# Kernel optimization log

Hardware: AMD Instinct MI355X
Metric: run time of the kernel (lower is better)

Reference implementation:

```python
import jax, jax.numpy as jnp
import numpy as np
import math

DIM = 128
K = 64
OUT = 256
N, H, W = 32, 64, 64
EPS = 1e-12  # F.normalize clamp


def _l2norm(v, axis):
    n = jnp.sqrt(jnp.sum(v * v, axis=axis, keepdims=True))
    return v / jnp.maximum(n, EPS)


def setup_inputs() -> dict:
    key = jax.random.key(0)
    ks = jax.random.split(key, 6)
    s = 1.0 / math.sqrt(DIM)
    x = jax.random.normal(ks[0], (N, DIM, H, W), dtype=jnp.float32)
    cluster_centers = jax.random.uniform(ks[1], (K, DIM), dtype=jnp.float32) * s
    conv_w = jax.random.normal(ks[2], (K, DIM), dtype=jnp.float32) * s  # 1x1 conv kernel squeezed
    conv_b = jax.random.normal(ks[3], (K,), dtype=jnp.float32) * s
    mlp_w = jax.random.normal(ks[4], (OUT, K * DIM), dtype=jnp.float32) * s / math.sqrt(K * DIM)
    mlp_b = jax.random.normal(ks[5], (OUT,), dtype=jnp.float32) * s
    return {"x": x, "cluster_centers": cluster_centers, "conv_w": conv_w,
            "conv_b": conv_b, "mlp_w": mlp_w, "mlp_b": mlp_b}


def reference(x, cluster_centers, conv_w, conv_b, mlp_w, mlp_b):
    n, c, h, w = x.shape
    xf = x.reshape(n, c, h * w)                                   # [N,C,P]
    # 1x1 conv == per-pixel matmul
    logits = jnp.einsum('kc,ncp->nkp', conv_w, xf) + conv_b[None, :, None]
    a = jax.nn.softmax(logits, axis=1)                            # softmax over clusters, [N,K,P]
    # VLAD via algebraic identity (same math as broadcast-subtract-sum):
    # sum_p a[n,k,p]*(x[n,c,p] - centers[k,c])
    vlad = jnp.einsum('nkp,ncp->nkc', a, xf) \
           - a.sum(axis=-1)[..., None] * cluster_centers[None]    # [N,K,C]
    vlad = _l2norm(vlad, axis=2)            # intra-normalization over C
    vlad = vlad.reshape(n, -1)              # [N, K*C]
    vlad = _l2norm(vlad, axis=1)
    vlad = vlad @ mlp_w.T + mlp_b           # [N, OUT]
    vlad = _l2norm(vlad, axis=1)
    return vlad
```

## Files before the change

kernel.cpp:

```cpp
#include <hip/hip_runtime.h>
#include <math.h>


#define N_IMG 32
#define C_DIM 128
#define P_PIX 4096
#define K_CL  64
#define OUT_D 256

#define CHUNKS 8
#define NSUB 4
#define PART_ROW 132
#define PART_BLK (K_CL * PART_ROW)

typedef __attribute__((ext_vector_type(8))) short bf16x8;
typedef __attribute__((ext_vector_type(4))) short bf16x4;
typedef __attribute__((ext_vector_type(4))) float f32x4;
typedef __attribute__((ext_vector_type(2))) unsigned u32x2;
typedef __attribute__((ext_vector_type(4))) unsigned u32x4;

__device__ __forceinline__ unsigned cvtpk(float a, float b) {
    unsigned r;
    asm("v_cvt_pk_bf16_f32 %0, %1, %2" : "=v"(r) : "v"(a), "v"(b));
    return r;
}
__device__ __forceinline__ unsigned short bf1(float a) {
    union { float f; unsigned u; } x; x.f = a;
    return (unsigned short)((x.u + 0x7FFFu + ((x.u >> 16) & 1u)) >> 16);
}

__device__ __forceinline__ f32x4 mfma16(bf16x8 a, bf16x8 b, f32x4 c) {
    return __builtin_amdgcn_mfma_f32_16x16x32_bf16(a, b, c, 0, 0, 0);
}

__device__ __forceinline__ u32x2 tr16(unsigned addr) {
    u32x2 d;
    asm volatile("ds_read_b64_tr_b16 %0, %1" : "=v"(d) : "v"(addr));
    return d;
}
__device__ __forceinline__ u32x2 tr16_o1024(unsigned addr) {
    u32x2 d;
    asm volatile("ds_read_b64_tr_b16 %0, %1 offset:1024" : "=v"(d) : "v"(addr));
    return d;
}

__device__ __forceinline__ void bar_lgkm() {
    __builtin_amdgcn_sched_barrier(0);
    asm volatile("s_waitcnt lgkmcnt(0)" ::: "memory");
    __builtin_amdgcn_s_barrier();
    __builtin_amdgcn_sched_barrier(0);
}

template<int CTRL>
__device__ __forceinline__ float dppmv(float v) {
    union { float f; int i; } u; u.f = v;
    u.i = __builtin_amdgcn_update_dpp(u.i, u.i, CTRL, 0xF, 0xF, false);
    return u.f;
}
__device__ __forceinline__ float rowmax16(float v) {
    v = fmaxf(v, dppmv<0xB1>(v));
    v = fmaxf(v, dppmv<0x4E>(v));
    v = fmaxf(v, dppmv<0x141>(v));
    v = fmaxf(v, dppmv<0x140>(v));
    return v;
}
__device__ __forceinline__ float rowsum16(float v) {
    v += dppmv<0xB1>(v);
    v += dppmv<0x4E>(v);
    v += dppmv<0x141>(v);
    v += dppmv<0x140>(v);
    return v;
}

__global__ __launch_bounds__(256, 1)
void k_vlad_mfma(const float* __restrict__ x, const float* __restrict__ conv_w,
                 const float* __restrict__ conv_b, float* __restrict__ part)
{
    __shared__ short xc_s[16384];
    __shared__ short a_s[8192];
    __shared__ short w_s[8192];
    __shared__ float asred[256];

    const int t   = threadIdx.x;
    const int w   = t >> 6;
    const int l   = t & 63;
    const int l15 = l & 15;
    const int lg  = l >> 4;
    const int n   = blockIdx.x >> 3;
    const int ch  = blockIdx.x & 7;
    const int pb0 = ch * 512;

    const unsigned xc_base = (unsigned)(unsigned long long)(void*)xc_s;
    const float LOG2E = 1.44269504f;

    const float* xr0 = x + ((long)n * C_DIM + 32 * w + l15) * P_PIX;
    const float* xr1 = xr0 + 16 * P_PIX;
    float4 raw[16];
#pragma unroll
    for (int h = 0; h < 2; ++h) {
        const float* xr = h ? xr1 : xr0;
#pragma unroll
        for (int ks = 0; ks < 4; ++ks) {
            const float* p = xr + pb0 + ks * 32 + lg * 8;
            raw[(h * 4 + ks) * 2 + 0] = *(const float4*)(p);
            raw[(h * 4 + ks) * 2 + 1] = *(const float4*)(p + 4);
        }
    }

    {
        const int k = t >> 2, quad = t & 3;
        const float* wr = conv_w + k * C_DIM + quad * 32;
#pragma unroll
        for (int j = 0; j < 4; ++j) {
            float4 a = *(const float4*)(wr + j * 8);
            float4 b = *(const float4*)(wr + j * 8 + 4);
            union { u32x4 u; bf16x8 v; } cv;
            cv.u.x = cvtpk(a.x * LOG2E, a.y * LOG2E);
            cv.u.y = cvtpk(a.z * LOG2E, a.w * LOG2E);
            cv.u.z = cvtpk(b.x * LOG2E, b.y * LOG2E);
            cv.u.w = cvtpk(b.z * LOG2E, b.w * LOG2E);
            const int g = quad * 4 + j;
            const unsigned off = (unsigned)(k * 256 + ((g * 16) ^ ((k & 7) << 4)));
            *(bf16x8*)((char*)w_s + off) = cv.v;
        }
    }
    float bias[4];
#pragma unroll
    for (int nt = 0; nt < 4; ++nt) bias[nt] = conv_b[nt * 16 + l15] * LOG2E;

    f32x4 acc2[4][2];
#pragma unroll
    for (int mt = 0; mt < 4; ++mt)
#pragma unroll
        for (int h = 0; h < 2; ++h)
            acc2[mt][h] = (f32x4){0.f, 0.f, 0.f, 0.f};
    float asum[4] = {0.f, 0.f, 0.f, 0.f};
    bf16x8 oct[2][4];

#pragma unroll
    for (int s = 0; s < NSUB; ++s) {
#pragma unroll
        for (int h = 0; h < 2; ++h)
#pragma unroll
            for (int ks = 0; ks < 4; ++ks) {
                const float4 A = raw[(h * 4 + ks) * 2];
                const float4 B = raw[(h * 4 + ks) * 2 + 1];
                union { u32x4 u; bf16x8 v; } cv;
                cv.u.x = cvtpk(A.x, A.y); cv.u.y = cvtpk(A.z, A.w);
                cv.u.z = cvtpk(B.x, B.y); cv.u.w = cvtpk(B.z, B.w);
                oct[h][ks] = cv.v;
            }
#pragma unroll
        for (int h = 0; h < 2; ++h)
#pragma unroll
            for (int ks = 0; ks < 4; ++ks) {
                const int c  = 32 * w + 16 * h + l15;
                const int pl = ks * 32 + lg * 8;
                const unsigned off = (unsigned)((c >> 2) * 1024 + (pl >> 4) * 128
                                                + (c & 3) * 32 + (pl & 15) * 2);
                *(bf16x8*)((char*)xc_s + off) = oct[h][ks];
            }
        if (s + 1 < NSUB) {
#pragma unroll
            for (int h = 0; h < 2; ++h) {
                const float* xr = h ? xr1 : xr0;
#pragma unroll
                for (int ks = 0; ks < 4; ++ks) {
                    const float* p = xr + pb0 + (s + 1) * 128 + ks * 32 + lg * 8;
                    raw[(h * 4 + ks) * 2 + 0] = *(const float4*)(p);
                    raw[(h * 4 + ks) * 2 + 1] = *(const float4*)(p + 4);
                }
            }
        }
        bar_lgkm();

        f32x4 acc1[2][4];
#pragma unroll
        for (int pt2 = 0; pt2 < 2; ++pt2)
#pragma unroll
            for (int nt = 0; nt < 4; ++nt)
                acc1[pt2][nt] = (f32x4){0.f, 0.f, 0.f, 0.f};
#pragma unroll
        for (int ks = 0; ks < 4; ++ks) {
            const unsigned ab = xc_base
                + (unsigned)((ks * 8 + lg * 2) * 1024 + l15 * 2);
            u32x2 t00 = tr16(ab + (2 * w + 0) * 128);
            u32x2 t01 = tr16_o1024(ab + (2 * w + 0) * 128);
            u32x2 t10 = tr16(ab + (2 * w + 1) * 128);
            u32x2 t11 = tr16_o1024(ab + (2 * w + 1) * 128);
            bf16x8 wfr[4];
#pragma unroll
            for (int nt = 0; nt < 4; ++nt) {
                const unsigned wb = (unsigned)((nt * 16 + l15) * 256
                    + ((ks * 64 + lg * 16) ^ ((l15 & 7) << 4)));
                wfr[nt] = *(const bf16x8*)((char*)w_s + wb);
            }
            asm volatile("s_waitcnt lgkmcnt(0)" ::: "memory");
            __builtin_amdgcn_sched_barrier(0);
            union { u32x4 u; bf16x8 v; } a0, a1;
            a0.u = (u32x4){t00.x, t00.y, t01.x, t01.y};
            a1.u = (u32x4){t10.x, t10.y, t11.x, t11.y};
#pragma unroll
            for (int nt = 0; nt < 4; ++nt) {
                acc1[0][nt] = mfma16(a0.v, wfr[nt], acc1[0][nt]);
                acc1[1][nt] = mfma16(a1.v, wfr[nt], acc1[1][nt]);
            }
        }

#pragma unroll
        for (int pt2 = 0; pt2 < 2; ++pt2) {
#pragma unroll
            for (int r = 0; r < 4; ++r) {
                float v0 = acc1[pt2][0][r] + bias[0];
                float v1 = acc1[pt2][1][r] + bias[1];
                float v2 = acc1[pt2][2][r] + bias[2];
                float v3 = acc1[pt2][3][r] + bias[3];
                float m = fmaxf(fmaxf(v0, v1), fmaxf(v2, v3));
                m = rowmax16(m);
                v0 = exp2f(v0 - m); v1 = exp2f(v1 - m);
                v2 = exp2f(v2 - m); v3 = exp2f(v3 - m);
                float sm = (v0 + v1) + (v2 + v3);
                sm = rowsum16(sm);
                const float inv = __builtin_amdgcn_rcpf(sm);
                v0 *= inv; v1 *= inv; v2 *= inv; v3 *= inv;
                asum[0] += v0; asum[1] += v1; asum[2] += v2; asum[3] += v3;
                acc1[pt2][0][r] = v0; acc1[pt2][1][r] = v1;
                acc1[pt2][2][r] = v2; acc1[pt2][3][r] = v3;
            }
        }
#pragma unroll
        for (int pt2 = 0; pt2 < 2; ++pt2) {
            const int pbyte = (2 * w + pt2) * 32 + lg * 8;
#pragma unroll
            for (int nt = 0; nt < 4; ++nt) {
                const int k = nt * 16 + l15;
                union { u32x2 u; bf16x4 v; } pk4;
                pk4.u.x = cvtpk(acc1[pt2][nt][0], acc1[pt2][nt][1]);
                pk4.u.y = cvtpk(acc1[pt2][nt][2], acc1[pt2][nt][3]);
                const unsigned off =
                    (unsigned)(k * 256 + (pbyte ^ ((k & 7) << 4)));
                *(bf16x4*)((char*)a_s + off) = pk4.v;
            }
        }
        bar_lgkm();

#pragma unroll
        for (int ks = 0; ks < 4; ++ks) {
            bf16x8 af[4];
#pragma unroll
            for (int mt = 0; mt < 4; ++mt) {
                const int k = mt * 16 + l15;
                const unsigned off = (unsigned)(k * 256
                    + ((ks * 64 + lg * 16) ^ ((k & 7) << 4)));
                af[mt] = *(const bf16x8*)((char*)a_s + off);
            }
#pragma unroll
            for (int mt = 0; mt < 4; ++mt)
#pragma unroll
                for (int h = 0; h < 2; ++h)
                    acc2[mt][h] = mfma16(af[mt], oct[h][ks], acc2[mt][h]);
        }
    }

    const long pbase = (long)blockIdx.x * PART_BLK;
#pragma unroll
    for (int mt = 0; mt < 4; ++mt)
#pragma unroll
        for (int h = 0; h < 2; ++h) {
            const int c = 32 * w + 16 * h + l15;
#pragma unroll
            for (int r = 0; r < 4; ++r) {
                const int k = mt * 16 + lg * 4 + r;
                part[pbase + (long)k * PART_ROW + c] = acc2[mt][h][r];
            }
        }
#pragma unroll
    for (int nt = 0; nt < 4; ++nt) {
        float a = asum[nt];
        a += __shfl_xor(a, 16);
        a += __shfl_xor(a, 32);
        if (lg == 0) asred[w * 64 + nt * 16 + l15] = a;
    }
    __syncthreads();
    if (t < 64) {
        float a = asred[t] + asred[64 + t] + asred[128 + t] + asred[192 + t];
        part[pbase + (long)t * PART_ROW + 128] = a;
    }
}

__global__ __launch_bounds__(128)
void k_reduce_norm(const float* __restrict__ part, const float* __restrict__ centers,
                   unsigned short* __restrict__ vn16, float* __restrict__ rsq)
{
    const int b = blockIdx.x;
    const int n = b >> 6, k = b & 63;
    const int c = threadIdx.x;
    float acc = 0.f, as = 0.f;
#pragma unroll
    for (int ch = 0; ch < CHUNKS; ++ch) {
        const float* p = part + ((long)(n * CHUNKS + ch) * PART_BLK + k * PART_ROW);
        acc += p[c];
        as  += p[128];
    }
    const float v = fmaf(-as, centers[k * C_DIM + c], acc);
    float sq = v * v;
#pragma unroll
    for (int m = 1; m < 64; m <<= 1) sq += __shfl_xor(sq, m);
    __shared__ float red[2];
    if ((c & 63) == 0) red[c >> 6] = sq;
    __syncthreads();
    const float total = red[0] + red[1];
    const float s = 1.0f / fmaxf(sqrtf(total), 1e-12f);
    vn16[(long)n * 8192 + k * C_DIM + c] = bf1(v * s);
    if (c == 0) rsq[n * K_CL + k] = total * s * s;
}

__global__ __launch_bounds__(256)
void k_mlp_mfma(const unsigned short* __restrict__ vn16,
                const float* __restrict__ mlp_w, float* __restrict__ part2)
{
    __shared__ short wt[8192];
    __shared__ short vt[8192];

    const int t  = threadIdx.x;
    const int og = blockIdx.x & 7;
    const int jc = blockIdx.x >> 3;
    const int j0 = jc * 256;

    {
        const int r = t >> 3, sub = t & 7;
        const float* wp = mlp_w + (long)(og * 32 + r) * 8192 + j0;
#pragma unroll
        for (int i = 0; i < 8; ++i) {
            const int jl = i * 32 + sub * 4;
            float4 a = *(const float4*)(wp + jl);
            union { u32x2 u; bf16x4 v; } cv;
            cv.u.x = cvtpk(a.x, a.y);
            cv.u.y = cvtpk(a.z, a.w);
            const unsigned off = (unsigned)(r * 512 + ((jl * 2) ^ ((r & 7) << 4)));
            *(bf16x4*)((char*)wt + off) = cv.v;
        }
    }
    {
        const int r = t >> 3, sub = t & 7;
        const unsigned short* vp = vn16 + (long)r * 8192 + j0;
#pragma unroll
        for (int i = 0; i < 4; ++i) {
            const int jl = i * 64 + sub * 8;
            bf16x8 v = *(const bf16x8*)(vp + jl);
            const unsigned off = (unsigned)(r * 512 + ((jl * 2) ^ ((r & 7) << 4)));
            *(bf16x8*)((char*)vt + off) = v;
        }
    }
    __syncthreads();

    const int w = t >> 6, l = t & 63, l15 = l & 15, lg = l >> 4;
    const int mt = w >> 1, ot = w & 1;
    f32x4 acc = (f32x4){0.f, 0.f, 0.f, 0.f};
#pragma unroll
    for (int kk = 0; kk < 8; ++kk) {
        const int rowa = mt * 16 + l15;
        const int rowb = ot * 16 + l15;
        const int jb = (kk * 32 + lg * 8) * 2;
        bf16x8 af = *(const bf16x8*)((char*)vt
                        + (unsigned)(rowa * 512 + (jb ^ ((rowa & 7) << 4))));
        bf16x8 bf = *(const bf16x8*)((char*)wt
                        + (unsigned)(rowb * 512 + (jb ^ ((rowb & 7) << 4))));
        acc = mfma16(af, bf, acc);
    }
#pragma unroll
    for (int r = 0; r < 4; ++r) {
        const int nn = mt * 16 + lg * 4 + r;
        const int oo = og * 32 + ot * 16 + l15;
        part2[(long)nn * 8192 + jc * 256 + oo] = acc[r];
    }
}

__global__ __launch_bounds__(1024)
void k_finalize(const float* __restrict__ part2, const float* __restrict__ mlp_b,
                const float* __restrict__ rsq, float* __restrict__ out)
{
    __shared__ float psum[4][256];
    __shared__ float red[4];
    const int n = blockIdx.x;
    const int t = threadIdx.x;
    const int o = t & 255, q = t >> 8;

    float acc = 0.f;
#pragma unroll
    for (int j = 0; j < 8; ++j)
        acc += part2[(long)n * 8192 + (q * 8 + j) * 256 + o];
    psum[q][o] = acc;
    __syncthreads();

    float y = 0.f;
    if (q == 0) {
        float g = 0.f;
#pragma unroll
        for (int i = 0; i < 16; ++i) {
            const float4 r = *(const float4*)&rsq[n * K_CL + i * 4];
            g += r.x + r.y + r.z + r.w;
        }
        const float s = 1.0f / fmaxf(sqrtf(g), 1e-12f);
        const float tot = psum[0][o] + psum[1][o] + psum[2][o] + psum[3][o];
        y = fmaf(tot * s, 1.0f, mlp_b[o]);
        float sq = y * y;
#pragma unroll
        for (int m = 1; m < 64; m <<= 1) sq += __shfl_xor(sq, m);
        if ((o & 63) == 0) red[o >> 6] = sq;
    }
    __syncthreads();
    if (q == 0) {
        const float tot2 = red[0] + red[1] + red[2] + red[3];
        out[n * OUT_D + o] = y / fmaxf(sqrtf(tot2), 1e-12f);
    }
}

extern "C" void kernel_launch(void* const* d_in, const int* in_sizes, int n_in,
                              void* d_out, int out_size, void* d_ws, size_t ws_size,
                              hipStream_t stream)
{
    const float* x       = (const float*)d_in[0];
    const float* centers = (const float*)d_in[1];
    const float* conv_w  = (const float*)d_in[2];
    const float* conv_b  = (const float*)d_in[3];
    const float* mlp_w   = (const float*)d_in[4];
    const float* mlp_b   = (const float*)d_in[5];

    float* ws = (float*)d_ws;
    float* part = ws;
    unsigned short* vn16 = (unsigned short*)(part + 256 * PART_BLK);
    float* rsq   = (float*)(vn16 + 32 * 8192);
    float* part2 = rsq + 2048;

    k_vlad_mfma<<<dim3(256), dim3(256), 0, stream>>>(x, conv_w, conv_b, part);
    k_reduce_norm<<<dim3(2048), dim3(128), 0, stream>>>(part, centers, vn16, rsq);
    k_mlp_mfma<<<dim3(256), dim3(256), 0, stream>>>(vn16, mlp_w, part2);
    k_finalize<<<dim3(32), dim3(1024), 0, stream>>>(part2, mlp_b, rsq, (float*)d_out);
}
```

Before: 38.06 us.

## Double wavefronts per block in VLAD kernel, halving per-wave channel and pixel work

The main VLAD kernel now runs 512 threads (8 waves) per block instead of 256. Each wave owns 16 channels and one 16-pixel tile rather than 32 channels and two tiles, so per-thread registers and MFMA chains shrink by half. The conv weight fragments are also loaded once into registers before the sub-chunk loop instead of being re-read from LDS every iteration. This is meant to raise latency hiding and occupancy for the global loads and MFMAs, at the cost of more waves contending at each barrier and higher register pressure from keeping the 16 preloaded weight fragments live.

```diff
diff --git a/kernel.cpp b/kernel.cpp
--- a/kernel.cpp
+++ b/kernel.cpp
@@ -72,14 +72,14 @@
     return v;
 }
 
-__global__ __launch_bounds__(256, 1)
+__global__ __launch_bounds__(512, 2)
 void k_vlad_mfma(const float* __restrict__ x, const float* __restrict__ conv_w,
                  const float* __restrict__ conv_b, float* __restrict__ part)
 {
     __shared__ short xc_s[16384];
     __shared__ short a_s[8192];
     __shared__ short w_s[8192];
-    __shared__ float asred[256];
+    __shared__ float asred[512];
 
     const int t   = threadIdx.x;
     const int w   = t >> 6;
@@ -93,25 +93,20 @@
     const unsigned xc_base = (unsigned)(unsigned long long)(void*)xc_s;
     const float LOG2E = 1.44269504f;
 
-    const float* xr0 = x + ((long)n * C_DIM + 32 * w + l15) * P_PIX;
-    const float* xr1 = xr0 + 16 * P_PIX;
-    float4 raw[16];
-#pragma unroll
-    for (int h = 0; h < 2; ++h) {
-        const float* xr = h ? xr1 : xr0;
-#pragma unroll
-        for (int ks = 0; ks < 4; ++ks) {
-            const float* p = xr + pb0 + ks * 32 + lg * 8;
-            raw[(h * 4 + ks) * 2 + 0] = *(const float4*)(p);
-            raw[(h * 4 + ks) * 2 + 1] = *(const float4*)(p + 4);
-        }
+    const float* xr0 = x + ((long)n * C_DIM + 16 * w + l15) * P_PIX;
+    float4 raw[8];
+#pragma unroll
+    for (int ks = 0; ks < 4; ++ks) {
+        const float* p = xr0 + pb0 + ks * 32 + lg * 8;
+        raw[ks * 2 + 0] = *(const float4*)(p);
+        raw[ks * 2 + 1] = *(const float4*)(p + 4);
     }
 
     {
-        const int k = t >> 2, quad = t & 3;
-        const float* wr = conv_w + k * C_DIM + quad * 32;
-#pragma unroll
-        for (int j = 0; j < 4; ++j) {
+        const int k = t >> 3, sub = t & 7;
+        const float* wr = conv_w + k * C_DIM + sub * 16;
+#pragma unroll
+        for (int j = 0; j < 2; ++j) {
             float4 a = *(const float4*)(wr + j * 8);
             float4 b = *(const float4*)(wr + j * 8 + 4);
             union { u32x4 u; bf16x8 v; } cv;
@@ -119,7 +114,7 @@
             cv.u.y = cvtpk(a.z * LOG2E, a.w * LOG2E);
             cv.u.z = cvtpk(b.x * LOG2E, b.y * LOG2E);
             cv.u.w = cvtpk(b.z * LOG2E, b.w * LOG2E);
-            const int g = quad * 4 + j;
+            const int g = sub * 2 + j;
             const unsigned off = (unsigned)(k * 256 + ((g * 16) ^ ((k & 7) << 4)));
             *(bf16x8*)((char*)w_s + off) = cv.v;
         }
@@ -128,115 +123,102 @@
 #pragma unroll
     for (int nt = 0; nt < 4; ++nt) bias[nt] = conv_b[nt * 16 + l15] * LOG2E;
 
-    f32x4 acc2[4][2];
-#pragma unroll
-    for (int mt = 0; mt < 4; ++mt)
-#pragma unroll
-        for (int h = 0; h < 2; ++h)
-            acc2[mt][h] = (f32x4){0.f, 0.f, 0.f, 0.f};
+    bar_lgkm();
+
+    bf16x8 wf[4][4];
+#pragma unroll
+    for (int nt = 0; nt < 4; ++nt)
+#pragma unroll
+        for (int ks = 0; ks < 4; ++ks) {
+            const unsigned wb = (unsigned)((nt * 16 + l15) * 256
+                + ((ks * 64 + lg * 16) ^ ((l15 & 7) << 4)));
+            wf[nt][ks] = *(const bf16x8*)((char*)w_s + wb);
+        }
+
+    f32x4 acc2[4];
+#pragma unroll
+    for (int mt = 0; mt < 4; ++mt) acc2[mt] = (f32x4){0.f, 0.f, 0.f, 0.f};
     float asum[4] = {0.f, 0.f, 0.f, 0.f};
-    bf16x8 oct[2][4];
+    bf16x8 oct[4];
 
 #pragma unroll
     for (int s = 0; s < NSUB; ++s) {
 #pragma unroll
-        for (int h = 0; h < 2; ++h)
+        for (int ks = 0; ks < 4; ++ks) {
+            const float4 A = raw[ks * 2];
+            const float4 B = raw[ks * 2 + 1];
+            union { u32x4 u; bf16x8 v; } cv;
+            cv.u.x = cvtpk(A.x, A.y); cv.u.y = cvtpk(A.z, A.w);
+            cv.u.z = cvtpk(B.x, B.y); cv.u.w = cvtpk(B.z, B.w);
+            oct[ks] = cv.v;
+        }
+#pragma unroll
+        for (int ks = 0; ks < 4; ++ks) {
+            const int c  = 16 * w + l15;
+            const int pl = ks * 32 + lg * 8;
+            const unsigned off = (unsigned)((c >> 2) * 1024 + (pl >> 4) * 128
+                                            + (c & 3) * 32 + (pl & 15) * 2);
+            *(bf16x8*)((char*)xc_s + off) = oct[ks];
+        }
+        if (s + 1 < NSUB) {
 #pragma unroll
             for (int ks = 0; ks < 4; ++ks) {
-                const float4 A = raw[(h * 4 + ks) * 2];
-                const float4 B = raw[(h * 4 + ks) * 2 + 1];
-                union { u32x4 u; bf16x8 v; } cv;
-                cv.u.x = cvtpk(A.x, A.y); cv.u.y = cvtpk(A.z, A.w);
-                cv.u.z = cvtpk(B.x, B.y); cv.u.w = cvtpk(B.z, B.w);
-                oct[h][ks] = cv.v;
+                const float* p = xr0 + pb0 + (s + 1) * 128 + ks * 32 + lg * 8;
+                raw[ks * 2 + 0] = *(const float4*)(p);
+                raw[ks * 2 + 1] = *(const float4*)(p + 4);
             }
-#pragma unroll
-        for (int h = 0; h < 2; ++h)
-#pragma unroll
-            for (int ks = 0; ks < 4; ++ks) {
-                const int c  = 32 * w + 16 * h + l15;
-                const int pl = ks * 32 + lg * 8;
-                const unsigned off = (unsigned)((c >> 2) * 1024 + (pl >> 4) * 128
-                                                + (c & 3) * 32 + (pl & 15) * 2);
-                *(bf16x8*)((char*)xc_s + off) = oct[h][ks];
-            }
-        if (s + 1 < NSUB) {
-#pragma unroll
-            for (int h = 0; h < 2; ++h) {
-                const float* xr = h ? xr1 : xr0;
-#pragma unroll
-                for (int ks = 0; ks < 4; ++ks) {
-                    const float* p = xr + pb0 + (s + 1) * 128 + ks * 32 + lg * 8;
-                    raw[(h * 4 + ks) * 2 + 0] = *(const float4*)(p);
-                    raw[(h * 4 + ks) * 2 + 1] = *(const float4*)(p + 4);
-                }
-            }
         }
         bar_lgkm();
 
-        f32x4 acc1[2][4];
-#pragma unroll
-        for (int pt2 = 0; pt2 < 2; ++pt2)
+        u32x2 trr[4][2];
+#pragma unroll
+        for (int ks = 0; ks < 4; ++ks) {
+            const unsigned ab = xc_base
+                + (unsigned)((ks * 8 + lg * 2) * 1024 + l15 * 2 + w * 128);
+            trr[ks][0] = tr16(ab);
+            trr[ks][1] = tr16_o1024(ab);
+        }
+        asm volatile("s_waitcnt lgkmcnt(0)" ::: "memory");
+        __builtin_amdgcn_sched_barrier(0);
+
+        f32x4 acc1[4];
+#pragma unroll
+        for (int nt = 0; nt < 4; ++nt) acc1[nt] = (f32x4){0.f, 0.f, 0.f, 0.f};
+#pragma unroll
+        for (int ks = 0; ks < 4; ++ks) {
+            union { u32x4 u; bf16x8 v; } a0;
+            a0.u = (u32x4){trr[ks][0].x, trr[ks][0].y, trr[ks][1].x, trr[ks][1].y};
 #pragma unroll
             for (int nt = 0; nt < 4; ++nt)
-                acc1[pt2][nt] = (f32x4){0.f, 0.f, 0.f, 0.f};
-#pragma unroll
-        for (int ks = 0; ks < 4; ++ks) {
-            const unsigned ab = xc_base
-                + (unsigned)((ks * 8 + lg * 2) * 1024 + l15 * 2);
-            u32x2 t00 = tr16(ab + (2 * w + 0) * 128);
-            u32x2 t01 = tr16_o1024(ab + (2 * w + 0) * 128);
-            u32x2 t10 = tr16(ab + (2 * w + 1) * 128);
-            u32x2 t11 = tr16_o1024(ab + (2 * w + 1) * 128);
-            bf16x8 wfr[4];
-#pragma unroll
-            for (int nt = 0; nt < 4; ++nt) {
-                const unsigned wb = (unsigned)((nt * 16 + l15) * 256
-                    + ((ks * 64 + lg * 16) ^ ((l15 & 7) << 4)));
-                wfr[nt] = *(const bf16x8*)((char*)w_s + wb);
-            }
-            asm volatile("s_waitcnt lgkmcnt(0)" ::: "memory");
-            __builtin_amdgcn_sched_barrier(0);
-            union { u32x4 u; bf16x8 v; } a0, a1;
-            a0.u = (u32x4){t00.x, t00.y, t01.x, t01.y};
-            a1.u = (u32x4){t10.x, t10.y, t11.x, t11.y};
-#pragma unroll
-            for (int nt = 0; nt < 4; ++nt) {
-                acc1[0][nt] = mfma16(a0.v, wfr[nt], acc1[0][nt]);
-                acc1[1][nt] = mfma16(a1.v, wfr[nt], acc1[1][nt]);
-            }
-        }
-
-#pragma unroll
-        for (int pt2 = 0; pt2 < 2; ++pt2) {
-#pragma unroll
-            for (int r = 0; r < 4; ++r) {
-                float v0 = acc1[pt2][0][r] + bias[0];
-                float v1 = acc1[pt2][1][r] + bias[1];
-                float v2 = acc1[pt2][2][r] + bias[2];
-                float v3 = acc1[pt2][3][r] + bias[3];
-                float m = fmaxf(fmaxf(v0, v1), fmaxf(v2, v3));
-                m = rowmax16(m);
-                v0 = exp2f(v0 - m); v1 = exp2f(v1 - m);
-                v2 = exp2f(v2 - m); v3 = exp2f(v3 - m);
-                float sm = (v0 + v1) + (v2 + v3);
-                sm = rowsum16(sm);
-                const float inv = __builtin_amdgcn_rcpf(sm);
-                v0 *= inv; v1 *= inv; v2 *= inv; v3 *= inv;
-                asum[0] += v0; asum[1] += v1; asum[2] += v2; asum[3] += v3;
-                acc1[pt2][0][r] = v0; acc1[pt2][1][r] = v1;
-                acc1[pt2][2][r] = v2; acc1[pt2][3][r] = v3;
-            }
-        }
-#pragma unroll
-        for (int pt2 = 0; pt2 < 2; ++pt2) {
-            const int pbyte = (2 * w + pt2) * 32 + lg * 8;
+                acc1[nt] = mfma16(a0.v, wf[nt][ks], acc1[nt]);
+        }
+
+#pragma unroll
+        for (int r = 0; r < 4; ++r) {
+            float v0 = acc1[0][r] + bias[0];
+            float v1 = acc1[1][r] + bias[1];
+            float v2 = acc1[2][r] + bias[2];
+            float v3 = acc1[3][r] + bias[3];
+            float m = fmaxf(fmaxf(v0, v1), fmaxf(v2, v3));
+            m = rowmax16(m);
+            v0 = exp2f(v0 - m); v1 = exp2f(v1 - m);
+            v2 = exp2f(v2 - m); v3 = exp2f(v3 - m);
+            float sm = (v0 + v1) + (v2 + v3);
+            sm = rowsum16(sm);
+            const float inv = __builtin_amdgcn_rcpf(sm);
+            v0 *= inv; v1 *= inv; v2 *= inv; v3 *= inv;
+            asum[0] += v0; asum[1] += v1; asum[2] += v2; asum[3] += v3;
+            acc1[0][r] = v0; acc1[1][r] = v1; acc1[2][r] = v2; acc1[3][r] = v3;
+        }
+
+        {
+            const int pbyte = w * 32 + lg * 8;
 #pragma unroll
             for (int nt = 0; nt < 4; ++nt) {
                 const int k = nt * 16 + l15;
                 union { u32x2 u; bf16x4 v; } pk4;
-                pk4.u.x = cvtpk(acc1[pt2][nt][0], acc1[pt2][nt][1]);
-                pk4.u.y = cvtpk(acc1[pt2][nt][2], acc1[pt2][nt][3]);
+                pk4.u.x = cvtpk(acc1[nt][0], acc1[nt][1]);
+                pk4.u.y = cvtpk(acc1[nt][2], acc1[nt][3]);
                 const unsigned off =
                     (unsigned)(k * 256 + (pbyte ^ ((k & 7) << 4)));
                 *(bf16x4*)((char*)a_s + off) = pk4.v;
@@ -256,24 +238,21 @@
             }
 #pragma unroll
             for (int mt = 0; mt < 4; ++mt)
-#pragma unroll
-                for (int h = 0; h < 2; ++h)
-                    acc2[mt][h] = mfma16(af[mt], oct[h][ks], acc2[mt][h]);
+                acc2[mt] = mfma16(af[mt], oct[ks], acc2[mt]);
         }
     }
 
     const long pbase = (long)blockIdx.x * PART_BLK;
-#pragma unroll
-    for (int mt = 0; mt < 4; ++mt)
-#pragma unroll
-        for (int h = 0; h < 2; ++h) {
-            const int c = 32 * w + 16 * h + l15;
+    {
+        const int c = 16 * w + l15;
+#pragma unroll
+        for (int mt = 0; mt < 4; ++mt)
 #pragma unroll
             for (int r = 0; r < 4; ++r) {
                 const int k = mt * 16 + lg * 4 + r;
-                part[pbase + (long)k * PART_ROW + c] = acc2[mt][h][r];
+                part[pbase + (long)k * PART_ROW + c] = acc2[mt][r];
             }
-        }
+    }
 #pragma unroll
     for (int nt = 0; nt < 4; ++nt) {
         float a = asum[nt];
@@ -283,7 +262,9 @@
     }
     __syncthreads();
     if (t < 64) {
-        float a = asred[t] + asred[64 + t] + asred[128 + t] + asred[192 + t];
+        float a = 0.f;
+#pragma unroll
+        for (int j = 0; j < 8; ++j) a += asred[j * 64 + t];
         part[pbase + (long)t * PART_ROW + 128] = a;
     }
 }
@@ -433,7 +414,7 @@
     float* rsq   = (float*)(vn16 + 32 * 8192);
     float* part2 = rsq + 2048;
 
-    k_vlad_mfma<<<dim3(256), dim3(256), 0, stream>>>(x, conv_w, conv_b, part);
+    k_vlad_mfma<<<dim3(256), dim3(512), 0, stream>>>(x, conv_w, conv_b, part);
     k_reduce_norm<<<dim3(2048), dim3(128), 0, stream>>>(part, centers, vn16, rsq);
     k_mlp_mfma<<<dim3(256), dim3(256), 0, stream>>>(vn16, mlp_w, part2);
     k_finalize<<<dim3(32), dim3(1024), 0, stream>>>(part2, mlp_b, rsq, (float*)d_out);
```

New measurement: 35.54 us. 1.07x faster.
